# Kernel tuning notes

Measured on AMD Instinct MI355X. Metric: run time of the kernel, lower is better.

Reference implementation:

```python
import jax, jax.numpy as jnp
import numpy as np

ALPHA = 1.0
DIAG_FILL = 500000.0


def _batch_pairwise_dist(x, y):
    # x: [B, Nx, D], y: [B, Ny, D] -> squared-distance matrix [B, Nx, Ny]
    xx = jnp.sum(x * x, axis=-1)  # [B, Nx]
    yy = jnp.sum(y * y, axis=-1)  # [B, Ny]
    zz = jnp.einsum('bnd,bmd->bnm', x, y)  # [B, Nx, Ny]
    return xx[:, :, None] + yy[:, None, :] - 2.0 * zz


def setup_inputs() -> dict:
    key = jax.random.key(0)
    k1, k2 = jax.random.split(key)
    B, N, D = 4, 4096, 3
    gts = jax.random.normal(k1, (B, N, D), dtype=jnp.float32)
    preds = jax.random.normal(k2, (B, N, D), dtype=jnp.float32)
    return {"gts": gts, "preds": preds}


def reference(gts, preds):
    # Cross-term Chamfer: P[b,i,j] = ||gts_i - preds_j||^2
    P = _batch_pairwise_dist(gts, preds)  # [B, Ng, Np]
    loss_1 = jnp.sum(jnp.min(P, axis=1), axis=1)  # min over gts, sum over preds
    loss_2 = jnp.sum(jnp.min(P, axis=2), axis=1)  # min over preds, sum over gts

    # Self nearest-neighbor distance distributions (diagonal masked out)
    Ng = gts.shape[1]
    Np = preds.shape[1]
    eye_g = jnp.eye(Ng, dtype=bool)
    eye_p = jnp.eye(Np, dtype=bool)
    P1 = jnp.where(eye_g[None, :, :], DIAG_FILL, _batch_pairwise_dist(gts, gts))
    P2 = jnp.where(eye_p[None, :, :], DIAG_FILL, _batch_pairwise_dist(preds, preds))

    mins1 = jnp.sort(jnp.min(P1, axis=1), axis=1)  # [B, Ng]
    mins2 = jnp.sort(jnp.min(P2, axis=1), axis=1)  # [B, Np]
    min_ps = min(mins1.shape[1], mins2.shape[1])
    loss_ordering = jnp.sum((mins1[:, :min_ps] - mins2[:, :min_ps]) ** 2, axis=1)

    return loss_1 + loss_2 + ALPHA * loss_ordering
```

## Files before the change

### kernel.cpp

```cpp
#include <hip/hip_runtime.h>

constexpr int BATCH = 4;
constexpr int NPTS  = 4096;
constexpr int TILE  = 128;
constexpr int NT    = NPTS / TILE;
constexpr int CROSS_TILES = NT * NT;
constexpr int TRI_TILES   = NT * (NT + 1) / 2;
constexpr int TILES_PER_BATCH = CROSS_TILES + 2 * TRI_TILES;


__global__ __launch_bounds__(256) void nn_init(unsigned int* __restrict__ m) {
    int i = blockIdx.x * blockDim.x + threadIdx.x;
    m[i] = 0x7F800000u;
}

__global__ __launch_bounds__(256) void nn_pass(const float* __restrict__ gts,
                                               const float* __restrict__ preds,
                                               unsigned int* __restrict__ nnmin) {
    const int b = blockIdx.y;
    int id = blockIdx.x;
    const float* A; const float* Bp;
    unsigned int* rowslot; unsigned int* colslot;
    int I, J;
    bool self;
    if (id < CROSS_TILES) {
        A = gts; Bp = preds;
        I = id >> 5; J = id & 31;
        rowslot = nnmin + ((size_t)0 * BATCH + b) * NPTS;
        colslot = nnmin + ((size_t)1 * BATCH + b) * NPTS;
        self = false;
    } else {
        id -= CROSS_TILES;
        const int which = id / TRI_TILES;
        int t = id - which * TRI_TILES;
        int i = 0;
        while (t >= NT - i) { t -= NT - i; ++i; }
        I = i; J = i + t;
        A = which ? preds : gts; Bp = A;
        rowslot = colslot = nnmin + ((size_t)(2 + which) * BATCH + b) * NPTS;
        self = true;
    }

    __shared__ float4 arow[TILE];
    __shared__ float4 bcol[TILE];
    __shared__ float  rp[TILE][17];
    __shared__ float  cp[TILE][17];

    const int tid = threadIdx.x;
    if (tid < TILE) {
        const float* p = A + ((size_t)b * NPTS + I * TILE + tid) * 3;
        arow[tid] = make_float4(p[0], p[1], p[2], 0.f);
    } else {
        const float* p = Bp + ((size_t)b * NPTS + J * TILE + (tid - TILE)) * 3;
        bcol[tid - TILE] = make_float4(p[0], p[1], p[2], 0.f);
    }
    __syncthreads();

    const int tx = tid & 15, ty = tid >> 4;
    float ax[8], ay[8], az[8], bx[8], by[8], bz[8];
#pragma unroll
    for (int r = 0; r < 8; ++r) {
        const float4 t = arow[ty * 8 + r];
        ax[r] = t.x; ay[r] = t.y; az[r] = t.z;
    }
#pragma unroll
    for (int c = 0; c < 8; ++c) {
        const float4 t = bcol[tx * 8 + c];
        bx[c] = t.x; by[c] = t.y; bz[c] = t.z;
    }

    float rmin[8], cmin[8];
#pragma unroll
    for (int r = 0; r < 8; ++r) { rmin[r] = 1e30f; cmin[r] = 1e30f; }

    const bool dt = self && (I == J) && (ty == tx);

#pragma unroll
    for (int r = 0; r < 8; ++r) {
#pragma unroll
        for (int c = 0; c < 8; ++c) {
            const float dx = ax[r] - bx[c];
            const float dy = ay[r] - by[c];
            const float dz = az[r] - bz[c];
            float d = fmaf(dz, dz, fmaf(dy, dy, dx * dx));
            if (r == c) d = dt ? 1e30f : d;
            rmin[r] = fminf(rmin[r], d);
            cmin[c] = fminf(cmin[c], d);
        }
    }

#pragma unroll
    for (int r = 0; r < 8; ++r) rp[ty * 8 + r][tx] = rmin[r];
#pragma unroll
    for (int c = 0; c < 8; ++c) cp[tx * 8 + c][ty] = cmin[c];
    __syncthreads();

    if (tid < TILE) {
        float m = rp[tid][0];
#pragma unroll
        for (int i = 1; i < 16; ++i) m = fminf(m, rp[tid][i]);
        atomicMin(&rowslot[I * TILE + tid], __float_as_uint(m));
    } else {
        const int t2 = tid - TILE;
        float m = cp[t2][0];
#pragma unroll
        for (int i = 1; i < 16; ++i) m = fminf(m, cp[t2][i]);
        atomicMin(&colslot[J * TILE + t2], __float_as_uint(m));
    }
}

__global__ __launch_bounds__(1024) void nn_sort(unsigned int* __restrict__ nnmin) {
    const int which = blockIdx.x & 1;
    const int b = blockIdx.x >> 1;
    unsigned int* src = nnmin + ((size_t)(2 + which) * BATCH + b) * NPTS;
    __shared__ float s[NPTS];
    const int tid = threadIdx.x;
    const int base = tid * 4;

    const uint4 u = reinterpret_cast<const uint4*>(src)[tid];
    float v[4] = {__uint_as_float(u.x), __uint_as_float(u.y),
                  __uint_as_float(u.z), __uint_as_float(u.w)};

    for (int k = 2; k <= NPTS; k <<= 1) {
        if (k >= 512) {
            s[base + 0] = v[0]; s[base + 1] = v[1]; s[base + 2] = v[2]; s[base + 3] = v[3];
            __syncthreads();
            for (int j = k >> 1; j >= 256; j >>= 1) {
#pragma unroll
                for (int tt = 0; tt < 2; ++tt) {
                    const int t = tid + tt * 1024;
                    const int i = ((t & ~(j - 1)) << 1) | (t & (j - 1));
                    const int p = i | j;
                    const bool asc = ((i & k) == 0);
                    const float a = s[i], c = s[p];
                    const float lo = fminf(a, c), hi = fmaxf(a, c);
                    s[i] = asc ? lo : hi;
                    s[p] = asc ? hi : lo;
                }
                __syncthreads();
            }
            v[0] = s[base + 0]; v[1] = s[base + 1]; v[2] = s[base + 2]; v[3] = s[base + 3];
        }
        for (int j = (k >> 1) > 128 ? 128 : (k >> 1); j >= 4; j >>= 1) {
            const int m = j >> 2;
#pragma unroll
            for (int e = 0; e < 4; ++e) {
                const float p = __shfl_xor(v[e], m, 64);
                const int i = base + e;
                const bool keepmin = (((i & j) == 0) == ((i & k) == 0));
                v[e] = keepmin ? fminf(v[e], p) : fmaxf(v[e], p);
            }
        }
        if (k >= 4) {
            const bool asc2 = ((base & k) == 0);
            float lo = fminf(v[0], v[2]), hi = fmaxf(v[0], v[2]);
            v[0] = asc2 ? lo : hi; v[2] = asc2 ? hi : lo;
            lo = fminf(v[1], v[3]); hi = fmaxf(v[1], v[3]);
            v[1] = asc2 ? lo : hi; v[3] = asc2 ? hi : lo;
        }
        {
            const bool ascA = (((base + 0) & k) == 0);
            const bool ascB = (((base + 2) & k) == 0);
            float lo = fminf(v[0], v[1]), hi = fmaxf(v[0], v[1]);
            v[0] = ascA ? lo : hi; v[1] = ascA ? hi : lo;
            lo = fminf(v[2], v[3]); hi = fmaxf(v[2], v[3]);
            v[2] = ascB ? lo : hi; v[3] = ascB ? hi : lo;
        }
    }

    reinterpret_cast<uint4*>(src)[tid] =
        make_uint4(__float_as_uint(v[0]), __float_as_uint(v[1]),
                   __float_as_uint(v[2]), __float_as_uint(v[3]));
}

__global__ __launch_bounds__(512) void nn_reduce(const unsigned int* __restrict__ nnmin,
                                                 float* __restrict__ out) {
    const int b = blockIdx.x;
    const int tid = threadIdx.x;
    __shared__ float red[512];

    const unsigned int* m0 = nnmin + ((size_t)0 * BATCH + b) * NPTS;
    const unsigned int* m1 = nnmin + ((size_t)1 * BATCH + b) * NPTS;
    const unsigned int* s1 = nnmin + ((size_t)2 * BATCH + b) * NPTS;
    const unsigned int* s2 = nnmin + ((size_t)3 * BATCH + b) * NPTS;

    float acc = 0.f;
    for (int i = tid; i < NPTS; i += 512) {
        acc += __uint_as_float(m0[i]) + __uint_as_float(m1[i]);
        const float d = __uint_as_float(s1[i]) - __uint_as_float(s2[i]);
        acc = fmaf(d, d, acc);
    }

    red[tid] = acc;
    __syncthreads();
    for (int s = 256; s > 0; s >>= 1) {
        if (tid < s) red[tid] += red[tid + s];
        __syncthreads();
    }
    if (tid == 0) out[b] = red[0];
}

extern "C" void kernel_launch(void* const* d_in, const int* in_sizes, int n_in,
                              void* d_out, int out_size, void* d_ws, size_t ws_size,
                              hipStream_t stream) {
    const float* gts   = (const float*)d_in[0];
    const float* preds = (const float*)d_in[1];
    float* out = (float*)d_out;
    unsigned int* nnmin = (unsigned int*)d_ws;

    nn_init<<<(4 * BATCH * NPTS) / 256, 256, 0, stream>>>(nnmin);
    dim3 grid(TILES_PER_BATCH, BATCH);
    nn_pass<<<grid, 256, 0, stream>>>(gts, preds, nnmin);
    nn_sort<<<2 * BATCH, 1024, 0, stream>>>(nnmin);
    nn_reduce<<<BATCH, 512, 0, stream>>>(nnmin, out);
}
```

Baseline: 125.9 us.

## Stream target chunks per query block, drop atomics, fuse sort with reduction

Replaces the symmetric tile-pair scheme with per-query-block kernels that stream all target chunks through double-buffered shared memory and compute row minima only, writing them directly without atomics or an init kernel. The two sorts and the final reduction are merged into one kernel that sorts both self-NN arrays together. This gives up the triangle symmetry and column-min reuse, roughly doubling distance evaluations, in exchange for fewer launches, no atomics and a lighter per-block prologue.

New measurement: 148.8 us. +18.2%, slower.

```diff
diff --git a/kernel.cpp b/kernel.cpp
--- a/kernel.cpp
+++ b/kernel.cpp
@@ -3,127 +3,143 @@
 constexpr int BATCH = 4;
 constexpr int NPTS  = 4096;
 constexpr int TILE  = 128;
-constexpr int NT    = NPTS / TILE;
-constexpr int CROSS_TILES = NT * NT;
-constexpr int TRI_TILES   = NT * (NT + 1) / 2;
-constexpr int TILES_PER_BATCH = CROSS_TILES + 2 * TRI_TILES;
-
-
-__global__ __launch_bounds__(256) void nn_init(unsigned int* __restrict__ m) {
-    int i = blockIdx.x * blockDim.x + threadIdx.x;
-    m[i] = 0x7F800000u;
+constexpr int NCH   = NPTS / TILE;
+constexpr int NTHR  = 512;
+
+
+__global__ __launch_bounds__(NTHR, 4) void nn_pass(const float* __restrict__ gts,
+                                                   const float* __restrict__ preds,
+                                                   float* __restrict__ nnmin) {
+    const int I    = blockIdx.x;
+    const int pass = blockIdx.y;
+    const int b    = blockIdx.z;
+    const float* __restrict__ A = (pass == 0 || pass == 2) ? gts : preds;
+    const float* __restrict__ T = (pass == 0 || pass == 3) ? preds : gts;
+    const bool self = pass >= 2;
+    float* __restrict__ slot = nnmin + ((size_t)pass * BATCH + b) * NPTS;
+
+    const int tid = threadIdx.x;
+    const int tx  = tid & 15;
+    const int ty  = tid >> 4;
+
+    const float* aptr = A + ((size_t)b * NPTS + I * TILE + ty * 4) * 3;
+    const float4 a0 = reinterpret_cast<const float4*>(aptr)[0];
+    const float4 a1 = reinterpret_cast<const float4*>(aptr)[1];
+    const float4 a2 = reinterpret_cast<const float4*>(aptr)[2];
+    const float ax[4] = {a0.x, a0.w, a1.z, a2.y};
+    const float ay[4] = {a0.y, a1.x, a1.w, a2.z};
+    const float az[4] = {a0.z, a1.y, a2.x, a2.w};
+
+    __shared__ float bst[2][3][192];
+
+    auto stage = [&](int ch, int buf) {
+        if (tid < 96) {
+            const float4 v = reinterpret_cast<const float4*>(
+                T + ((size_t)b * NPTS + ch * TILE) * 3)[tid];
+            const int f0 = tid * 4;
+#pragma unroll
+            for (int e = 0; e < 4; ++e) {
+                const int f = f0 + e;
+                const int p = f / 3, comp = f - 3 * p;
+                bst[buf][comp][12 * (p >> 3) + (p & 7)] = (&v.x)[e];
+            }
+        }
+    };
+
+    stage(0, 0);
+    __syncthreads();
+
+    float rmin[4] = {1e30f, 1e30f, 1e30f, 1e30f};
+
+    for (int ch = 0; ch < NCH; ++ch) {
+        const int buf = ch & 1;
+        if (ch + 1 < NCH) stage(ch + 1, buf ^ 1);
+
+        const float4 x0 = *(const float4*)&bst[buf][0][12 * tx];
+        const float4 x1 = *(const float4*)&bst[buf][0][12 * tx + 4];
+        const float4 y0 = *(const float4*)&bst[buf][1][12 * tx];
+        const float4 y1 = *(const float4*)&bst[buf][1][12 * tx + 4];
+        const float4 z0 = *(const float4*)&bst[buf][2][12 * tx];
+        const float4 z1 = *(const float4*)&bst[buf][2][12 * tx + 4];
+        const float bx[8] = {x0.x, x0.y, x0.z, x0.w, x1.x, x1.y, x1.z, x1.w};
+        const float by[8] = {y0.x, y0.y, y0.z, y0.w, y1.x, y1.y, y1.z, y1.w};
+        const float bz[8] = {z0.x, z0.y, z0.z, z0.w, z1.x, z1.y, z1.z, z1.w};
+
+        if (self && ch == I) {
+#pragma unroll
+            for (int r = 0; r < 4; ++r) {
+                const int lr = ty * 4 + r;
+#pragma unroll
+                for (int c = 0; c < 8; ++c) {
+                    const float dx = ax[r] - bx[c];
+                    const float dy = ay[r] - by[c];
+                    const float dz = az[r] - bz[c];
+                    float d = fmaf(dz, dz, fmaf(dy, dy, dx * dx));
+                    d = (lr == tx * 8 + c) ? 1e30f : d;
+                    rmin[r] = fminf(rmin[r], d);
+                }
+            }
+        } else {
+#pragma unroll
+            for (int r = 0; r < 4; ++r) {
+#pragma unroll
+                for (int c = 0; c < 8; ++c) {
+                    const float dx = ax[r] - bx[c];
+                    const float dy = ay[r] - by[c];
+                    const float dz = az[r] - bz[c];
+                    const float d = fmaf(dz, dz, fmaf(dy, dy, dx * dx));
+                    rmin[r] = fminf(rmin[r], d);
+                }
+            }
+        }
+        __syncthreads();
+    }
+
+#pragma unroll
+    for (int r = 0; r < 4; ++r) {
+        float m = rmin[r];
+        m = fminf(m, __shfl_xor(m, 1, 64));
+        m = fminf(m, __shfl_xor(m, 2, 64));
+        m = fminf(m, __shfl_xor(m, 4, 64));
+        m = fminf(m, __shfl_xor(m, 8, 64));
+        rmin[r] = m;
+    }
+    if (tx == 0) {
+#pragma unroll
+        for (int r = 0; r < 4; ++r)
+            slot[I * TILE + ty * 4 + r] = rmin[r];
+    }
 }
 
-__global__ __launch_bounds__(256) void nn_pass(const float* __restrict__ gts,
-                                               const float* __restrict__ preds,
-                                               unsigned int* __restrict__ nnmin) {
-    const int b = blockIdx.y;
-    int id = blockIdx.x;
-    const float* A; const float* Bp;
-    unsigned int* rowslot; unsigned int* colslot;
-    int I, J;
-    bool self;
-    if (id < CROSS_TILES) {
-        A = gts; Bp = preds;
-        I = id >> 5; J = id & 31;
-        rowslot = nnmin + ((size_t)0 * BATCH + b) * NPTS;
-        colslot = nnmin + ((size_t)1 * BATCH + b) * NPTS;
-        self = false;
-    } else {
-        id -= CROSS_TILES;
-        const int which = id / TRI_TILES;
-        int t = id - which * TRI_TILES;
-        int i = 0;
-        while (t >= NT - i) { t -= NT - i; ++i; }
-        I = i; J = i + t;
-        A = which ? preds : gts; Bp = A;
-        rowslot = colslot = nnmin + ((size_t)(2 + which) * BATCH + b) * NPTS;
-        self = true;
-    }
-
-    __shared__ float4 arow[TILE];
-    __shared__ float4 bcol[TILE];
-    __shared__ float  rp[TILE][17];
-    __shared__ float  cp[TILE][17];
-
+__global__ __launch_bounds__(1024) void nn_final(const float* __restrict__ nnmin,
+                                                 float* __restrict__ out) {
+    const int b   = blockIdx.x;
     const int tid = threadIdx.x;
-    if (tid < TILE) {
-        const float* p = A + ((size_t)b * NPTS + I * TILE + tid) * 3;
-        arow[tid] = make_float4(p[0], p[1], p[2], 0.f);
-    } else {
-        const float* p = Bp + ((size_t)b * NPTS + J * TILE + (tid - TILE)) * 3;
-        bcol[tid - TILE] = make_float4(p[0], p[1], p[2], 0.f);
-    }
-    __syncthreads();
-
-    const int tx = tid & 15, ty = tid >> 4;
-    float ax[8], ay[8], az[8], bx[8], by[8], bz[8];
-#pragma unroll
-    for (int r = 0; r < 8; ++r) {
-        const float4 t = arow[ty * 8 + r];
-        ax[r] = t.x; ay[r] = t.y; az[r] = t.z;
-    }
-#pragma unroll
-    for (int c = 0; c < 8; ++c) {
-        const float4 t = bcol[tx * 8 + c];
-        bx[c] = t.x; by[c] = t.y; bz[c] = t.z;
-    }
-
-    float rmin[8], cmin[8];
-#pragma unroll
-    for (int r = 0; r < 8; ++r) { rmin[r] = 1e30f; cmin[r] = 1e30f; }
-
-    const bool dt = self && (I == J) && (ty == tx);
-
-#pragma unroll
-    for (int r = 0; r < 8; ++r) {
-#pragma unroll
-        for (int c = 0; c < 8; ++c) {
-            const float dx = ax[r] - bx[c];
-            const float dy = ay[r] - by[c];
-            const float dz = az[r] - bz[c];
-            float d = fmaf(dz, dz, fmaf(dy, dy, dx * dx));
-            if (r == c) d = dt ? 1e30f : d;
-            rmin[r] = fminf(rmin[r], d);
-            cmin[c] = fminf(cmin[c], d);
-        }
-    }
-
-#pragma unroll
-    for (int r = 0; r < 8; ++r) rp[ty * 8 + r][tx] = rmin[r];
-#pragma unroll
-    for (int c = 0; c < 8; ++c) cp[tx * 8 + c][ty] = cmin[c];
-    __syncthreads();
-
-    if (tid < TILE) {
-        float m = rp[tid][0];
-#pragma unroll
-        for (int i = 1; i < 16; ++i) m = fminf(m, rp[tid][i]);
-        atomicMin(&rowslot[I * TILE + tid], __float_as_uint(m));
-    } else {
-        const int t2 = tid - TILE;
-        float m = cp[t2][0];
-#pragma unroll
-        for (int i = 1; i < 16; ++i) m = fminf(m, cp[t2][i]);
-        atomicMin(&colslot[J * TILE + t2], __float_as_uint(m));
-    }
-}
-
-__global__ __launch_bounds__(1024) void nn_sort(unsigned int* __restrict__ nnmin) {
-    const int which = blockIdx.x & 1;
-    const int b = blockIdx.x >> 1;
-    unsigned int* src = nnmin + ((size_t)(2 + which) * BATCH + b) * NPTS;
-    __shared__ float s[NPTS];
-    const int tid = threadIdx.x;
+    __shared__ float s[2][NPTS];
+    __shared__ float red[1024];
+
+    const float* m0 = nnmin + ((size_t)0 * BATCH + b) * NPTS;
+    const float* m1 = nnmin + ((size_t)1 * BATCH + b) * NPTS;
+    const float* q1 = nnmin + ((size_t)2 * BATCH + b) * NPTS;
+    const float* q2 = nnmin + ((size_t)3 * BATCH + b) * NPTS;
+
+    float acc;
+    {
+        const float4 c0 = ((const float4*)m0)[tid];
+        const float4 c1 = ((const float4*)m1)[tid];
+        acc = c0.x + c0.y + c0.z + c0.w + c1.x + c1.y + c1.z + c1.w;
+    }
+
+    const float4 u1 = ((const float4*)q1)[tid];
+    const float4 u2 = ((const float4*)q2)[tid];
+    float v1[4] = {u1.x, u1.y, u1.z, u1.w};
+    float v2[4] = {u2.x, u2.y, u2.z, u2.w};
     const int base = tid * 4;
-
-    const uint4 u = reinterpret_cast<const uint4*>(src)[tid];
-    float v[4] = {__uint_as_float(u.x), __uint_as_float(u.y),
-                  __uint_as_float(u.z), __uint_as_float(u.w)};
 
     for (int k = 2; k <= NPTS; k <<= 1) {
         if (k >= 512) {
-            s[base + 0] = v[0]; s[base + 1] = v[1]; s[base + 2] = v[2]; s[base + 3] = v[3];
+#pragma unroll
+            for (int e = 0; e < 4; ++e) { s[0][base + e] = v1[e]; s[1][base + e] = v2[e]; }
             __syncthreads();
             for (int j = k >> 1; j >= 256; j >>= 1) {
 #pragma unroll
@@ -132,69 +148,66 @@
                     const int i = ((t & ~(j - 1)) << 1) | (t & (j - 1));
                     const int p = i | j;
                     const bool asc = ((i & k) == 0);
-                    const float a = s[i], c = s[p];
-                    const float lo = fminf(a, c), hi = fmaxf(a, c);
-                    s[i] = asc ? lo : hi;
-                    s[p] = asc ? hi : lo;
+#pragma unroll
+                    for (int a = 0; a < 2; ++a) {
+                        const float A0 = s[a][i], C0 = s[a][p];
+                        const float lo = fminf(A0, C0), hi = fmaxf(A0, C0);
+                        s[a][i] = asc ? lo : hi;
+                        s[a][p] = asc ? hi : lo;
+                    }
                 }
                 __syncthreads();
             }
-            v[0] = s[base + 0]; v[1] = s[base + 1]; v[2] = s[base + 2]; v[3] = s[base + 3];
+#pragma unroll
+            for (int e = 0; e < 4; ++e) { v1[e] = s[0][base + e]; v2[e] = s[1][base + e]; }
         }
         for (int j = (k >> 1) > 128 ? 128 : (k >> 1); j >= 4; j >>= 1) {
             const int m = j >> 2;
 #pragma unroll
             for (int e = 0; e < 4; ++e) {
-                const float p = __shfl_xor(v[e], m, 64);
                 const int i = base + e;
                 const bool keepmin = (((i & j) == 0) == ((i & k) == 0));
-                v[e] = keepmin ? fminf(v[e], p) : fmaxf(v[e], p);
+                const float p1 = __shfl_xor(v1[e], m, 64);
+                v1[e] = keepmin ? fminf(v1[e], p1) : fmaxf(v1[e], p1);
+                const float p2 = __shfl_xor(v2[e], m, 64);
+                v2[e] = keepmin ? fminf(v2[e], p2) : fmaxf(v2[e], p2);
             }
         }
         if (k >= 4) {
             const bool asc2 = ((base & k) == 0);
-            float lo = fminf(v[0], v[2]), hi = fmaxf(v[0], v[2]);
-            v[0] = asc2 ? lo : hi; v[2] = asc2 ? hi : lo;
-            lo = fminf(v[1], v[3]); hi = fmaxf(v[1], v[3]);
-            v[1] = asc2 ? lo : hi; v[3] = asc2 ? hi : lo;
+            float lo = fminf(v1[0], v1[2]), hi = fmaxf(v1[0], v1[2]);
+            v1[0] = asc2 ? lo : hi; v1[2] = asc2 ? hi : lo;
+            lo = fminf(v1[1], v1[3]); hi = fmaxf(v1[1], v1[3]);
+            v1[1] = asc2 ? lo : hi; v1[3] = asc2 ? hi : lo;
+            lo = fminf(v2[0], v2[2]); hi = fmaxf(v2[0], v2[2]);
+            v2[0] = asc2 ? lo : hi; v2[2] = asc2 ? hi : lo;
+            lo = fminf(v2[1], v2[3]); hi = fmaxf(v2[1], v2[3]);
+            v2[1] = asc2 ? lo : hi; v2[3] = asc2 ? hi : lo;
         }
         {
             const bool ascA = (((base + 0) & k) == 0);
             const bool ascB = (((base + 2) & k) == 0);
-            float lo = fminf(v[0], v[1]), hi = fmaxf(v[0], v[1]);
-            v[0] = ascA ? lo : hi; v[1] = ascA ? hi : lo;
-            lo = fminf(v[2], v[3]); hi = fmaxf(v[2], v[3]);
-            v[2] = ascB ? lo : hi; v[3] = ascB ? hi : lo;
-        }
-    }
-
-    reinterpret_cast<uint4*>(src)[tid] =
-        make_uint4(__float_as_uint(v[0]), __float_as_uint(v[1]),
-                   __float_as_uint(v[2]), __float_as_uint(v[3]));
-}
-
-__global__ __launch_bounds__(512) void nn_reduce(const unsigned int* __restrict__ nnmin,
-                                                 float* __restrict__ out) {
-    const int b = blockIdx.x;
-    const int tid = threadIdx.x;
-    __shared__ float red[512];
-
-    const unsigned int* m0 = nnmin + ((size_t)0 * BATCH + b) * NPTS;
-    const unsigned int* m1 = nnmin + ((size_t)1 * BATCH + b) * NPTS;
-    const unsigned int* s1 = nnmin + ((size_t)2 * BATCH + b) * NPTS;
-    const unsigned int* s2 = nnmin + ((size_t)3 * BATCH + b) * NPTS;
-
-    float acc = 0.f;
-    for (int i = tid; i < NPTS; i += 512) {
-        acc += __uint_as_float(m0[i]) + __uint_as_float(m1[i]);
-        const float d = __uint_as_float(s1[i]) - __uint_as_float(s2[i]);
+            float lo = fminf(v1[0], v1[1]), hi = fmaxf(v1[0], v1[1]);
+            v1[0] = ascA ? lo : hi; v1[1] = ascA ? hi : lo;
+            lo = fminf(v1[2], v1[3]); hi = fmaxf(v1[2], v1[3]);
+            v1[2] = ascB ? lo : hi; v1[3] = ascB ? hi : lo;
+            lo = fminf(v2[0], v2[1]); hi = fmaxf(v2[0], v2[1]);
+            v2[0] = ascA ? lo : hi; v2[1] = ascA ? hi : lo;
+            lo = fminf(v2[2], v2[3]); hi = fmaxf(v2[2], v2[3]);
+            v2[2] = ascB ? lo : hi; v2[3] = ascB ? hi : lo;
+        }
+    }
+
+#pragma unroll
+    for (int e = 0; e < 4; ++e) {
+        const float d = v1[e] - v2[e];
         acc = fmaf(d, d, acc);
     }
 
     red[tid] = acc;
     __syncthreads();
-    for (int s = 256; s > 0; s >>= 1) {
-        if (tid < s) red[tid] += red[tid + s];
+    for (int sft = 512; sft > 0; sft >>= 1) {
+        if (tid < sft) red[tid] += red[tid + sft];
         __syncthreads();
     }
     if (tid == 0) out[b] = red[0];
@@ -205,12 +218,10 @@
                               hipStream_t stream) {
     const float* gts   = (const float*)d_in[0];
     const float* preds = (const float*)d_in[1];
-    float* out = (float*)d_out;
-    unsigned int* nnmin = (unsigned int*)d_ws;
-
-    nn_init<<<(4 * BATCH * NPTS) / 256, 256, 0, stream>>>(nnmin);
-    dim3 grid(TILES_PER_BATCH, BATCH);
-    nn_pass<<<grid, 256, 0, stream>>>(gts, preds, nnmin);
-    nn_sort<<<2 * BATCH, 1024, 0, stream>>>(nnmin);
-    nn_reduce<<<BATCH, 512, 0, stream>>>(nnmin, out);
+    float* out   = (float*)d_out;
+    float* nnmin = (float*)d_ws;
+
+    dim3 grid(NCH, 4, BATCH);
+    nn_pass<<<grid, NTHR, 0, stream>>>(gts, preds, nnmin);
+    nn_final<<<BATCH, 1024, 0, stream>>>(nnmin, out);
 }
```
